# Kernel optimization log

Hardware: AMD Instinct MI355X
Metric: run time of the kernel (lower is better)

Reference implementation:

```python
import jax, jax.numpy as jnp
import numpy as np

D_MODEL = 1024
N_HEADS = 16
D_K = D_MODEL // N_HEADS
B, L = 4, 2048


def setup_inputs() -> dict:
    key = jax.random.key(0)
    ks = jax.random.split(key, 9)
    s = 1.0 / np.sqrt(D_MODEL)
    return {
        "x": jax.random.normal(ks[0], (B, L, D_MODEL), dtype=jnp.float32),
        "Wq": jax.random.normal(ks[1], (D_MODEL, D_MODEL), dtype=jnp.float32) * s,
        "bq": jax.random.normal(ks[2], (D_MODEL,), dtype=jnp.float32) * 0.01,
        "Wk": jax.random.normal(ks[3], (D_MODEL, D_MODEL), dtype=jnp.float32) * s,
        "bk": jax.random.normal(ks[4], (D_MODEL,), dtype=jnp.float32) * 0.01,
        "Wv": jax.random.normal(ks[5], (D_MODEL, D_MODEL), dtype=jnp.float32) * s,
        "bv": jax.random.normal(ks[6], (D_MODEL,), dtype=jnp.float32) * 0.01,
        "Wo": jax.random.normal(ks[7], (D_MODEL, D_MODEL), dtype=jnp.float32) * s,
        "bo": jax.random.normal(ks[8], (D_MODEL,), dtype=jnp.float32) * 0.01,
    }


def reference(x, Wq, bq, Wk, bk, Wv, bv, Wo, bo):
    b, l, d = x.shape
    scale = jnp.asarray(np.sqrt(D_K), x.dtype)
    # project and split heads: [B, H, L, d_k]
    def heads(w, bias):
        p = x @ w.T + bias
        return p.reshape(b, l, N_HEADS, D_K).transpose(0, 2, 1, 3)
    Q = heads(Wq, bq)
    K = heads(Wk, bk)
    V = heads(Wv, bv)
    scores = jnp.einsum("bhqd,bhkd->bhqk", Q, K) / scale
    scores = jnp.clip(scores, -100.0, 100.0)
    attn = jax.nn.softmax(scores, axis=-1)  # dropout is identity in eval
    ctx = jnp.einsum("bhqk,bhkd->bhqd", attn, V)
    ctx = ctx.transpose(0, 2, 1, 3).reshape(b, l, d)
    return ctx @ Wo.T + bo
```

## Files before the change

### kernel.cpp

```cpp
#include <hip/hip_runtime.h>
#include <stdint.h>

#define L_SEQ   2048
#define DM      1024
#define NH      16
#define DK      64
#define BATCH   4
#define M_TOK   (BATCH * L_SEQ)

typedef __attribute__((ext_vector_type(8))) short bf16x8;
typedef __attribute__((ext_vector_type(4))) float f32x4;
typedef __attribute__((ext_vector_type(16))) float f32x16;
typedef __attribute__((ext_vector_type(4))) unsigned int u32x4;

typedef __attribute__((address_space(1))) void void_g;
typedef __attribute__((address_space(3))) void void_l;

#define EXP2F(x) __builtin_amdgcn_exp2f(x)

__device__ __forceinline__ unsigned short f2bf(float f) {
  unsigned int u = __builtin_bit_cast(unsigned int, f);
  u += 0x7FFFu + ((u >> 16) & 1u);
  return (unsigned short)(u >> 16);
}

__global__ void cvt_f32_bf16(const float* __restrict__ src,
                             unsigned short* __restrict__ dst, int n4) {
  int i = blockIdx.x * blockDim.x + threadIdx.x;
  int stride = gridDim.x * blockDim.x;
  for (; i < n4; i += stride) {
    float4 v = ((const float4*)src)[i];
    ushort4 o;
    o.x = f2bf(v.x); o.y = f2bf(v.y); o.z = f2bf(v.z); o.w = f2bf(v.w);
    ((ushort4*)dst)[i] = o;
  }
}

__global__ void cvt_w4(const float* __restrict__ s0, const float* __restrict__ s1,
                       const float* __restrict__ s2, const float* __restrict__ s3,
                       unsigned short* __restrict__ dst) {
  int i = blockIdx.x * blockDim.x + threadIdx.x;
  int sel = i >> 18, j = i & 0x3FFFF;
  const float* s = sel == 0 ? s0 : sel == 1 ? s1 : sel == 2 ? s2 : s3;
  float4 v = ((const float4*)s)[j];
  ushort4 o;
  o.x = f2bf(v.x); o.y = f2bf(v.y); o.z = f2bf(v.z); o.w = f2bf(v.w);
  ((ushort4*)(dst + (size_t)sel * DM * DM))[j] = o;
}

#define GBK 32
#define NKT (DM / GBK)
#define AT32 (128 * GBK)

template <int NW, int NCH>
__device__ __forceinline__ void stage32(
    const unsigned short* __restrict__ S, unsigned short* buf,
    int row0, int k0, int t) {
  const int l = t & 63, w = t >> 6;
  const int su = (l & 3) ^ ((l >> 3) & 3);
  const int rl = l >> 2;
#pragma unroll
  for (int r = 0; r < NCH / NW; ++r) {
    const int c = r * NW + w;
    __builtin_amdgcn_global_load_lds(
        (const void_g*)(S + (size_t)(row0 + c * 16 + rl) * DM + k0 + su * 8),
        (void_l*)(buf + c * 512), 16, 0, 0);
  }
}

__device__ __forceinline__ bf16x8 frag_ld32(const unsigned short* base, int R, int u) {
  return *(const bf16x8*)(base + R * 32 + ((u ^ ((R >> 1) & 3)) * 8));
}

template <int EPI, int BN_, int NW>
__global__ __launch_bounds__(NW * 64, 3) void gemm8(
    const unsigned short* __restrict__ A,
    const unsigned short* __restrict__ Bw,
    const float* __restrict__ b0, const float* __restrict__ b1,
    const float* __restrict__ b2, float qscale,
    void* __restrict__ out) {
  constexpr int BUFE = (128 + BN_) * GBK;
  constexpr int BCH = BN_ / 16;
  __shared__ unsigned short L[3 * BUFE];

  const int tidx = threadIdx.x;
  const int wid = tidx >> 6, lane = tidx & 63;
  constexpr int WN = NW / 2;
  const int wm = wid / WN, wn = wid % WN;
  const int lr = lane & 15, lg4 = lane >> 4;

  int wg = blockIdx.y * gridDim.x + blockIdx.x;
  int nwg = gridDim.x * gridDim.y;
  int swz = (wg & 7) * (nwg >> 3) + (wg >> 3);
  const int tm = (swz / gridDim.x) * 128, tn = (swz % gridDim.x) * BN_;

  f32x4 acc[4][4];
#pragma unroll
  for (int m = 0; m < 4; ++m)
#pragma unroll
    for (int n = 0; n < 4; ++n) acc[m][n] = (f32x4)0.0f;

  stage32<NW, 8>(A, L, tm, 0, tidx);
  stage32<NW, BCH>(Bw, L + AT32, tn, 0, tidx);
  stage32<NW, 8>(A, L + BUFE, tm, GBK, tidx);
  stage32<NW, BCH>(Bw, L + BUFE + AT32, tn, GBK, tidx);
  asm volatile("s_waitcnt vmcnt(4)" ::: "memory");
  __builtin_amdgcn_s_barrier();

  for (int i = 0; i < NKT; ++i) {
    unsigned short* cb = L + (i % 3) * BUFE;
    unsigned short* nb = L + ((i + 2) % 3) * BUFE;
    const bool pf = (i + 2 < NKT);

    bf16x8 a[4], b[4];
#pragma unroll
    for (int m = 0; m < 4; ++m)
      a[m] = frag_ld32(cb, wm * 64 + m * 16 + lr, lg4);
#pragma unroll
    for (int n = 0; n < 4; ++n)
      b[n] = frag_ld32(cb + AT32, wn * 64 + n * 16 + lr, lg4);

    if (pf) {
      stage32<NW, 8>(A, nb, tm, (i + 2) * GBK, tidx);
      stage32<NW, BCH>(Bw, nb + AT32, tn, (i + 2) * GBK, tidx);
    }

    asm volatile("s_waitcnt lgkmcnt(0)" ::: "memory");
    __builtin_amdgcn_s_setprio(1);
#pragma unroll
    for (int m = 0; m < 4; ++m)
#pragma unroll
      for (int n = 0; n < 4; ++n)
        acc[m][n] = __builtin_amdgcn_mfma_f32_16x16x32_bf16(a[m], b[n], acc[m][n], 0, 0, 0);
    __builtin_amdgcn_s_setprio(0);

    if (pf) asm volatile("s_waitcnt vmcnt(4)" ::: "memory");
    else    asm volatile("s_waitcnt vmcnt(0)" ::: "memory");
    __builtin_amdgcn_s_barrier();
  }

  if (EPI == 1) {
    float* o = (float*)out;
#pragma unroll
    for (int m = 0; m < 4; ++m) {
      int row0 = tm + wm * 64 + m * 16 + lg4 * 4;
#pragma unroll
      for (int n = 0; n < 4; ++n) {
        int col = tn + wn * 64 + n * 16 + lr;
        float bc = b0[col];
#pragma unroll
        for (int jj = 0; jj < 4; ++jj)
          o[(size_t)(row0 + jj) * DM + col] = acc[m][n][jj] + bc;
      }
    }
  } else {
    const int sel = tn >> 10;
    const float* bias = sel == 0 ? b0 : sel == 1 ? b1 : b2;
    const float scl = sel == 0 ? qscale : 1.0f;
    unsigned short* dst = (unsigned short*)out + (size_t)sel * (8u << 20);
    unsigned short* C = L;
    const int bb = tm >> 11, l0 = tm & 2047;
    const int tnl = tn & 1023;
    constexpr int LST = BN_ + 8;
    constexpr int CPR = BN_ / 8;
    constexpr int ITR = 128 * CPR / (NW * 64);

    if (sel < 2) {
#pragma unroll
      for (int m = 0; m < 4; ++m) {
        int row0 = wm * 64 + m * 16 + lg4 * 4;
#pragma unroll
        for (int n = 0; n < 4; ++n) {
          int col = wn * 64 + n * 16 + lr;
          float bc = bias[tnl + col];
#pragma unroll
          for (int jj = 0; jj < 4; ++jj)
            C[(row0 + jj) * LST + col] = f2bf((acc[m][n][jj] + bc) * scl);
        }
      }
      __syncthreads();
#pragma unroll
      for (int j = 0; j < ITR; ++j) {
        int c = j * NW * 64 + tidx;
        int ll = c / CPR, colc = (c % CPR) * 8;
        bf16x8 v = *(const bf16x8*)&C[ll * LST + colc];
        int c10 = tnl + colc;
        int h = c10 >> 6, dd = c10 & 63;
        *(bf16x8*)&dst[(((size_t)bb * NH + h) * L_SEQ + (l0 + ll)) * DK + dd] = v;
      }
    } else {
#pragma unroll
      for (int m = 0; m < 4; ++m) {
        int row0 = wm * 64 + m * 16 + lg4 * 4;
#pragma unroll
        for (int n = 0; n < 4; ++n) {
          int col = wn * 64 + n * 16 + lr;
          float bc = bias[tnl + col];
          ushort4 pk;
          pk.x = f2bf(acc[m][n][0] + bc);
          pk.y = f2bf(acc[m][n][1] + bc);
          pk.z = f2bf(acc[m][n][2] + bc);
          pk.w = f2bf(acc[m][n][3] + bc);
          *(ushort4*)&C[col * 136 + row0] = pk;
        }
      }
      __syncthreads();
      constexpr int ITV = BN_ * 16 / (NW * 64);
#pragma unroll
      for (int j = 0; j < ITV; ++j) {
        int c = j * NW * 64 + tidx;
        int ddl = c >> 4, tk = (c & 15) * 8;
        bf16x8 v = *(const bf16x8*)&C[ddl * 136 + tk];
        int c10 = tnl + ddl;
        int h = c10 >> 6, dd = c10 & 63;
        *(bf16x8*)&dst[(((size_t)bb * NH + h) * DK + dd) * L_SEQ + (l0 + tk)] = v;
      }
    }
  }
}

#define KVB 64
#define LDK 68
#define NTILE (L_SEQ / KVB)
#define FIXM  32.0f

__device__ __forceinline__ bf16x8 lds_frag(const unsigned short* p) {
  uint2 a = *(const uint2*)p;
  uint2 b = *(const uint2*)(p + 4);
  u32x4 t = {a.x, a.y, b.x, b.y};
  return __builtin_bit_cast(bf16x8, t);
}

__device__ __forceinline__ void lds_st16(unsigned short* p, uint4 v) {
  *(uint2*)p = make_uint2(v.x, v.y);
  *(uint2*)(p + 4) = make_uint2(v.z, v.w);
}

__device__ __forceinline__ unsigned cvtpk(float a, float b) {
  unsigned r;
  asm("v_cvt_pk_bf16_f32 %0, %1, %2" : "=v"(r) : "v"(a), "v"(b));
  return r;
}

__device__ __forceinline__ void pl32swap(unsigned& a, unsigned& b) {
  unsigned sa = (unsigned)__shfl_xor((int)a, 32);
  unsigned sb = (unsigned)__shfl_xor((int)b, 32);
  int hi = (threadIdx.x & 63) >> 5;
  unsigned na = hi ? sb : a;
  unsigned nb = hi ? b : sa;
  a = na; b = nb;
}

__device__ __forceinline__ void xpair32(float x, float& lo, float& hi2) {
  unsigned a = __builtin_bit_cast(unsigned, x), b = a;
  pl32swap(a, b);
  lo = __builtin_bit_cast(float, a);
  hi2 = __builtin_bit_cast(float, b);
}

#define MFMA32(a, b, c) __builtin_amdgcn_mfma_f32_32x32x16_bf16(a, b, c, 0, 0, 0)

__global__ __launch_bounds__(256, 4) void flash_attn(
    const unsigned short* __restrict__ Qg,
    const unsigned short* __restrict__ Kg,
    const unsigned short* __restrict__ VTg,
    unsigned short* __restrict__ ctx) {
  __shared__ unsigned short Ks[2][64 * LDK];
  __shared__ unsigned short Vs[2][64 * LDK];

  const int bh = blockIdx.x, b = bh >> 4, h = bh & 15;
  const int q0 = blockIdx.y * 128;
  const int tid = threadIdx.x;
  const int w = tid >> 6, lane = tid & 63;
  const int l31 = lane & 31, hi = lane >> 5;
  const size_t head = (size_t)bh * (L_SEQ * DK);

  const int srow = w * 16 + (lane >> 2);
  const int scol = (lane & 3) * 16;

  bf16x8 qf[4];
  {
    const unsigned short* qp = Qg + head + (size_t)(q0 + w * 32 + l31) * DK + hi * 8;
#pragma unroll
    for (int ks = 0; ks < 4; ++ks) qf[ks] = *(const bf16x8*)(qp + ks * 16);
  }

  f32x16 o[2];
  o[0] = (f32x16)0.0f; o[1] = (f32x16)0.0f;
  float lq = 0.0f;

  {
    const unsigned short* kp = Kg + head + (size_t)srow * DK + scol;
    uint4 k0 = *(const uint4*)kp, k1 = *(const uint4*)(kp + 8);
    const unsigned short* vp = VTg + head + (size_t)srow * L_SEQ + scol;
    uint4 v0 = *(const uint4*)vp, v1 = *(const uint4*)(vp + 8);
    lds_st16(Ks[0] + srow * LDK + scol, k0);
    lds_st16(Ks[0] + srow * LDK + scol + 8, k1);
    lds_st16(Vs[0] + srow * LDK + scol, v0);
    lds_st16(Vs[0] + srow * LDK + scol + 8, v1);
  }
  __syncthreads();

  int cur = 0;
  for (int t = 0; t < NTILE; ++t) {
    uint4 kr0, kr1, vr0, vr1;
    const int kv0n = (t + 1) * KVB;
    if (t + 1 < NTILE) {
      const unsigned short* kp = Kg + head + (size_t)(kv0n + srow) * DK + scol;
      kr0 = *(const uint4*)kp; kr1 = *(const uint4*)(kp + 8);
    }

    f32x16 s0 = (f32x16)(-FIXM), s1 = (f32x16)(-FIXM);
#pragma unroll
    for (int ks = 0; ks < 4; ++ks) {
      bf16x8 k0 = lds_frag(Ks[cur] + l31 * LDK + ks * 16 + hi * 8);
      s0 = MFMA32(k0, qf[ks], s0);
      bf16x8 k1 = lds_frag(Ks[cur] + (32 + l31) * LDK + ks * 16 + hi * 8);
      s1 = MFMA32(k1, qf[ks], s1);
    }

#pragma unroll
    for (int r = 0; r < 16; ++r) {
      s0[r] = EXP2F(s0[r]);
      s1[r] = EXP2F(s1[r]);
    }
    {
      float l4[4];
#pragma unroll
      for (int r = 0; r < 4; ++r)
        l4[r] = ((s0[r] + s0[r + 4]) + (s0[r + 8] + s0[r + 12]))
              + ((s1[r] + s1[r + 4]) + (s1[r + 8] + s1[r + 12]));
      lq += (l4[0] + l4[1]) + (l4[2] + l4[3]);
    }

    bf16x8 pa[4];
#pragma unroll
    for (int ks = 0; ks < 4; ++ks) {
      const int s8 = (ks & 1) * 8;
      const f32x16 sv = (ks < 2) ? s0 : s1;
      unsigned uA0 = cvtpk(sv[s8 + 0], sv[s8 + 1]);
      unsigned uA1 = cvtpk(sv[s8 + 2], sv[s8 + 3]);
      unsigned uB0 = cvtpk(sv[s8 + 4], sv[s8 + 5]);
      unsigned uB1 = cvtpk(sv[s8 + 6], sv[s8 + 7]);
      pl32swap(uA0, uB0);
      pl32swap(uA1, uB1);
      u32x4 tt = {uA0, uA1, uB0, uB1};
      pa[ks] = __builtin_bit_cast(bf16x8, tt);
    }

    if (t + 1 < NTILE) {
      const unsigned short* vp = VTg + head + (size_t)srow * L_SEQ + kv0n + scol;
      vr0 = *(const uint4*)vp; vr1 = *(const uint4*)(vp + 8);
    }

#pragma unroll
    for (int jb = 0; jb < 2; ++jb)
#pragma unroll
      for (int ks = 0; ks < 4; ++ks) {
        bf16x8 vf = lds_frag(Vs[cur] + (32 * jb + l31) * LDK + ks * 16 + hi * 8);
        o[jb] = MFMA32(vf, pa[ks], o[jb]);
      }

    if (t + 1 < NTILE) {
      lds_st16(Ks[cur ^ 1] + srow * LDK + scol, kr0);
      lds_st16(Ks[cur ^ 1] + srow * LDK + scol + 8, kr1);
      lds_st16(Vs[cur ^ 1] + srow * LDK + scol, vr0);
      lds_st16(Vs[cur ^ 1] + srow * LDK + scol + 8, vr1);
    }
    __syncthreads();
    cur ^= 1;
  }

  {
    float a, c;
    xpair32(lq, a, c);
    float inv = 1.0f / (a + c);
    const int tok = q0 + w * 32 + l31;
    size_t base = ((size_t)b * L_SEQ + tok) * DM + h * DK;
#pragma unroll
    for (int jb = 0; jb < 2; ++jb)
#pragma unroll
      for (int c2 = 0; c2 < 4; ++c2) {
        ushort4 pk;
        pk.x = f2bf(o[jb][4 * c2 + 0] * inv);
        pk.y = f2bf(o[jb][4 * c2 + 1] * inv);
        pk.z = f2bf(o[jb][4 * c2 + 2] * inv);
        pk.w = f2bf(o[jb][4 * c2 + 3] * inv);
        *(ushort4*)&ctx[base + jb * 32 + c2 * 8 + hi * 4] = pk;
      }
  }
}

extern "C" void kernel_launch(void* const* d_in, const int* in_sizes, int n_in,
                              void* d_out, int out_size, void* d_ws, size_t ws_size,
                              hipStream_t stream) {
  (void)in_sizes; (void)n_in; (void)out_size; (void)ws_size;
  const float* x  = (const float*)d_in[0];
  const float* Wq = (const float*)d_in[1];
  const float* bq = (const float*)d_in[2];
  const float* Wk = (const float*)d_in[3];
  const float* bk = (const float*)d_in[4];
  const float* Wv = (const float*)d_in[5];
  const float* bv = (const float*)d_in[6];
  const float* Wo = (const float*)d_in[7];
  const float* bo = (const float*)d_in[8];

  char* ws = (char*)d_ws;
  unsigned short* xb  = (unsigned short*)(ws);
  unsigned short* wqb = (unsigned short*)(ws + (16ull << 20));
  unsigned short* wob = (unsigned short*)(ws + (22ull << 20));
  unsigned short* Qb  = (unsigned short*)(ws + (24ull << 20));
  unsigned short* Kb  = (unsigned short*)(ws + (40ull << 20));
  unsigned short* VTb = (unsigned short*)(ws + (56ull << 20));
  unsigned short* ctx = xb;

  cvt_f32_bf16<<<2048, 256, 0, stream>>>(x, xb, M_TOK * DM / 4);
  cvt_w4<<<4096, 256, 0, stream>>>(Wq, Wk, Wv, Wo, wqb);

  gemm8<0, 128, 4><<<dim3(3 * DM / 128, M_TOK / 128), 256, 0, stream>>>(
      xb, wqb, bq, bk, bv, 0.1803368801f, Qb);

  dim3 ga(BATCH * NH, L_SEQ / 128);
  flash_attn<<<ga, 256, 0, stream>>>(Qb, Kb, VTb, ctx);

  gemm8<1, 128, 4><<<dim3(DM / 128, M_TOK / 128), 256, 0, stream>>>(
      ctx, wob, bo, nullptr, nullptr, 1.0f, d_out);
}
```

Before: 195.7 us.

## Double query rows per attention wave and widen QKV GEMM tile

The flash attention kernel now processes 256 query rows per block, 64 per wave as two 32-row sub-tiles. This lets each K fragment loaded from LDS and each V fragment be reused across two MFMA chains, halving K/V LDS traffic and global K/V reloads per query. The QKV projection GEMM switches to 128x256 tiles with 8 waves, and its vmcnt waits are adjusted for the different staging count. The cost is higher register pressure (launch bounds drop to 2 blocks per SM for attention) and half as many attention blocks, which may reduce occupancy and latency hiding.

```diff
diff --git a/kernel.cpp b/kernel.cpp
--- a/kernel.cpp
+++ b/kernel.cpp
@@ -73,7 +73,7 @@
 }
 
 template <int EPI, int BN_, int NW>
-__global__ __launch_bounds__(NW * 64, 3) void gemm8(
+__global__ __launch_bounds__(NW * 64, EPI == 0 ? 4 : 3) void gemm8(
     const unsigned short* __restrict__ A,
     const unsigned short* __restrict__ Bw,
     const float* __restrict__ b0, const float* __restrict__ b1,
@@ -104,7 +104,8 @@
   stage32<NW, BCH>(Bw, L + AT32, tn, 0, tidx);
   stage32<NW, 8>(A, L + BUFE, tm, GBK, tidx);
   stage32<NW, BCH>(Bw, L + BUFE + AT32, tn, GBK, tidx);
-  asm volatile("s_waitcnt vmcnt(4)" ::: "memory");
+  if constexpr (EPI == 0) asm volatile("s_waitcnt vmcnt(3)" ::: "memory");
+  else                    asm volatile("s_waitcnt vmcnt(4)" ::: "memory");
   __builtin_amdgcn_s_barrier();
 
   for (int i = 0; i < NKT; ++i) {
@@ -134,8 +135,12 @@
         acc[m][n] = __builtin_amdgcn_mfma_f32_16x16x32_bf16(a[m], b[n], acc[m][n], 0, 0, 0);
     __builtin_amdgcn_s_setprio(0);
 
-    if (pf) asm volatile("s_waitcnt vmcnt(4)" ::: "memory");
-    else    asm volatile("s_waitcnt vmcnt(0)" ::: "memory");
+    if (pf) {
+      if constexpr (EPI == 0) asm volatile("s_waitcnt vmcnt(3)" ::: "memory");
+      else                    asm volatile("s_waitcnt vmcnt(4)" ::: "memory");
+    } else {
+      asm volatile("s_waitcnt vmcnt(0)" ::: "memory");
+    }
     __builtin_amdgcn_s_barrier();
   }
 
@@ -260,7 +265,7 @@
 
 #define MFMA32(a, b, c) __builtin_amdgcn_mfma_f32_32x32x16_bf16(a, b, c, 0, 0, 0)
 
-__global__ __launch_bounds__(256, 4) void flash_attn(
+__global__ __launch_bounds__(256, 2) void flash_attn(
     const unsigned short* __restrict__ Qg,
     const unsigned short* __restrict__ Kg,
     const unsigned short* __restrict__ VTg,
@@ -269,7 +274,7 @@
   __shared__ unsigned short Vs[2][64 * LDK];
 
   const int bh = blockIdx.x, b = bh >> 4, h = bh & 15;
-  const int q0 = blockIdx.y * 128;
+  const int q0 = blockIdx.y * 256;
   const int tid = threadIdx.x;
   const int w = tid >> 6, lane = tid & 63;
   const int l31 = lane & 31, hi = lane >> 5;
@@ -278,16 +283,21 @@
   const int srow = w * 16 + (lane >> 2);
   const int scol = (lane & 3) * 16;
 
-  bf16x8 qf[4];
-  {
-    const unsigned short* qp = Qg + head + (size_t)(q0 + w * 32 + l31) * DK + hi * 8;
-#pragma unroll
-    for (int ks = 0; ks < 4; ++ks) qf[ks] = *(const bf16x8*)(qp + ks * 16);
-  }
-
-  f32x16 o[2];
-  o[0] = (f32x16)0.0f; o[1] = (f32x16)0.0f;
-  float lq = 0.0f;
+  bf16x8 qf[2][4];
+#pragma unroll
+  for (int qq = 0; qq < 2; ++qq) {
+    const unsigned short* qp = Qg + head + (size_t)(q0 + w * 64 + qq * 32 + l31) * DK + hi * 8;
+#pragma unroll
+    for (int ks = 0; ks < 4; ++ks) qf[qq][ks] = *(const bf16x8*)(qp + ks * 16);
+  }
+
+  f32x16 o[2][2];
+#pragma unroll
+  for (int qq = 0; qq < 2; ++qq) {
+    o[qq][0] = (f32x16)0.0f;
+    o[qq][1] = (f32x16)0.0f;
+  }
+  float lq[2] = {0.0f, 0.0f};
 
   {
     const unsigned short* kp = Kg + head + (size_t)srow * DK + scol;
@@ -310,42 +320,48 @@
       kr0 = *(const uint4*)kp; kr1 = *(const uint4*)(kp + 8);
     }
 
-    f32x16 s0 = (f32x16)(-FIXM), s1 = (f32x16)(-FIXM);
-#pragma unroll
-    for (int ks = 0; ks < 4; ++ks) {
-      bf16x8 k0 = lds_frag(Ks[cur] + l31 * LDK + ks * 16 + hi * 8);
-      s0 = MFMA32(k0, qf[ks], s0);
-      bf16x8 k1 = lds_frag(Ks[cur] + (32 + l31) * LDK + ks * 16 + hi * 8);
-      s1 = MFMA32(k1, qf[ks], s1);
-    }
-
-#pragma unroll
-    for (int r = 0; r < 16; ++r) {
-      s0[r] = EXP2F(s0[r]);
-      s1[r] = EXP2F(s1[r]);
-    }
-    {
-      float l4[4];
-#pragma unroll
-      for (int r = 0; r < 4; ++r)
-        l4[r] = ((s0[r] + s0[r + 4]) + (s0[r + 8] + s0[r + 12]))
-              + ((s1[r] + s1[r + 4]) + (s1[r + 8] + s1[r + 12]));
-      lq += (l4[0] + l4[1]) + (l4[2] + l4[3]);
-    }
-
-    bf16x8 pa[4];
-#pragma unroll
-    for (int ks = 0; ks < 4; ++ks) {
-      const int s8 = (ks & 1) * 8;
-      const f32x16 sv = (ks < 2) ? s0 : s1;
-      unsigned uA0 = cvtpk(sv[s8 + 0], sv[s8 + 1]);
-      unsigned uA1 = cvtpk(sv[s8 + 2], sv[s8 + 3]);
-      unsigned uB0 = cvtpk(sv[s8 + 4], sv[s8 + 5]);
-      unsigned uB1 = cvtpk(sv[s8 + 6], sv[s8 + 7]);
-      pl32swap(uA0, uB0);
-      pl32swap(uA1, uB1);
-      u32x4 tt = {uA0, uA1, uB0, uB1};
-      pa[ks] = __builtin_bit_cast(bf16x8, tt);
+    bf16x8 kf[2][4];
+#pragma unroll
+    for (int m = 0; m < 2; ++m)
+#pragma unroll
+      for (int ks = 0; ks < 4; ++ks)
+        kf[m][ks] = lds_frag(Ks[cur] + (32 * m + l31) * LDK + ks * 16 + hi * 8);
+
+    bf16x8 pa[2][4];
+#pragma unroll
+    for (int qq = 0; qq < 2; ++qq) {
+      f32x16 s0 = (f32x16)(-FIXM), s1 = (f32x16)(-FIXM);
+#pragma unroll
+      for (int ks = 0; ks < 4; ++ks) {
+        s0 = MFMA32(kf[0][ks], qf[qq][ks], s0);
+        s1 = MFMA32(kf[1][ks], qf[qq][ks], s1);
+      }
+#pragma unroll
+      for (int r = 0; r < 16; ++r) {
+        s0[r] = EXP2F(s0[r]);
+        s1[r] = EXP2F(s1[r]);
+      }
+      {
+        float l4[4];
+#pragma unroll
+        for (int r = 0; r < 4; ++r)
+          l4[r] = ((s0[r] + s0[r + 4]) + (s0[r + 8] + s0[r + 12]))
+                + ((s1[r] + s1[r + 4]) + (s1[r + 8] + s1[r + 12]));
+        lq[qq] += (l4[0] + l4[1]) + (l4[2] + l4[3]);
+      }
+#pragma unroll
+      for (int ks = 0; ks < 4; ++ks) {
+        const int s8 = (ks & 1) * 8;
+        const f32x16 sv = (ks < 2) ? s0 : s1;
+        unsigned uA0 = cvtpk(sv[s8 + 0], sv[s8 + 1]);
+        unsigned uA1 = cvtpk(sv[s8 + 2], sv[s8 + 3]);
+        unsigned uB0 = cvtpk(sv[s8 + 4], sv[s8 + 5]);
+        unsigned uB1 = cvtpk(sv[s8 + 6], sv[s8 + 7]);
+        pl32swap(uA0, uB0);
+        pl32swap(uA1, uB1);
+        u32x4 tt = {uA0, uA1, uB0, uB1};
+        pa[qq][ks] = __builtin_bit_cast(bf16x8, tt);
+      }
     }
 
     if (t + 1 < NTILE) {
@@ -358,7 +374,8 @@
 #pragma unroll
       for (int ks = 0; ks < 4; ++ks) {
         bf16x8 vf = lds_frag(Vs[cur] + (32 * jb + l31) * LDK + ks * 16 + hi * 8);
-        o[jb] = MFMA32(vf, pa[ks], o[jb]);
+        o[0][jb] = MFMA32(vf, pa[0][ks], o[0][jb]);
+        o[1][jb] = MFMA32(vf, pa[1][ks], o[1][jb]);
       }
 
     if (t + 1 < NTILE) {
@@ -371,21 +388,22 @@
     cur ^= 1;
   }
 
-  {
+#pragma unroll
+  for (int qq = 0; qq < 2; ++qq) {
     float a, c;
-    xpair32(lq, a, c);
+    xpair32(lq[qq], a, c);
     float inv = 1.0f / (a + c);
-    const int tok = q0 + w * 32 + l31;
+    const int tok = q0 + w * 64 + qq * 32 + l31;
     size_t base = ((size_t)b * L_SEQ + tok) * DM + h * DK;
 #pragma unroll
     for (int jb = 0; jb < 2; ++jb)
 #pragma unroll
       for (int c2 = 0; c2 < 4; ++c2) {
         ushort4 pk;
-        pk.x = f2bf(o[jb][4 * c2 + 0] * inv);
-        pk.y = f2bf(o[jb][4 * c2 + 1] * inv);
-        pk.z = f2bf(o[jb][4 * c2 + 2] * inv);
-        pk.w = f2bf(o[jb][4 * c2 + 3] * inv);
+        pk.x = f2bf(o[qq][jb][4 * c2 + 0] * inv);
+        pk.y = f2bf(o[qq][jb][4 * c2 + 1] * inv);
+        pk.z = f2bf(o[qq][jb][4 * c2 + 2] * inv);
+        pk.w = f2bf(o[qq][jb][4 * c2 + 3] * inv);
         *(ushort4*)&ctx[base + jb * 32 + c2 * 8 + hi * 4] = pk;
       }
   }
@@ -417,10 +435,10 @@
   cvt_f32_bf16<<<2048, 256, 0, stream>>>(x, xb, M_TOK * DM / 4);
   cvt_w4<<<4096, 256, 0, stream>>>(Wq, Wk, Wv, Wo, wqb);
 
-  gemm8<0, 128, 4><<<dim3(3 * DM / 128, M_TOK / 128), 256, 0, stream>>>(
+  gemm8<0, 256, 8><<<dim3(3 * DM / 256, M_TOK / 128), 512, 0, stream>>>(
       xb, wqb, bq, bk, bv, 0.1803368801f, Qb);
 
-  dim3 ga(BATCH * NH, L_SEQ / 128);
+  dim3 ga(BATCH * NH, L_SEQ / 256);
   flash_attn<<<ga, 256, 0, stream>>>(Qb, Kb, VTb, ctx);
 
   gemm8<1, 128, 4><<<dim3(DM / 128, M_TOK / 128), 256, 0, stream>>>(
```

After: 187.5 us. -4.2%, faster.
